# Kernel tuning notes

Hardware: AMD Instinct MI355X
Metric: run time of the kernel (lower is better)

Reference implementation:

```python
import jax, jax.numpy as jnp
import numpy as np

B, N = 32, 320          # n_graphs, max_num_nodes
MAX_DIST = 10
NUM_HEADS = 8
AVG_DEG = 8.0


def setup_inputs() -> dict:
    key = jax.random.key(0)
    k1, k2, k3 = jax.random.split(key, 3)
    # random sparse symmetric adjacency, no self loops
    a = jax.random.uniform(k1, (B, N, N)) < (AVG_DEG / N)
    adj = (a | jnp.swapaxes(a, 1, 2)) & ~jnp.eye(N, dtype=bool)[None]
    num_nodes = jax.random.randint(k2, (B,), N // 2 + 1, N + 1).astype(jnp.int32)
    emb_table = jax.random.normal(k3, (MAX_DIST + 2, NUM_HEADS), dtype=jnp.float32)
    emb_table = emb_table.at[0].set(0.0)  # padding_idx=0 (dist == -1 rows)
    return {"adj": adj, "num_nodes": num_nodes, "emb_table": emb_table}


def _batched_apsp(adj, num_nodes, max_dist):
    """Batched all-pairs shortest path distance via parallel frontier BFS.

    adj: [B,N,N] bool, num_nodes: [B] int. Returns dist [B,N,N] int32 with
    -1 for unreachable/padded pairs; reachable dists > max_dist are set to
    max_dist (equivalent after the clamp in the spatial encoder).
    """
    Bn, Nn, _ = adj.shape
    valid = jnp.arange(Nn)[None, :] < num_nodes[:, None]        # [B,N]
    pair = valid[:, :, None] & valid[:, None, :]                # [B,N,N]
    adj = adj & pair
    eye = jnp.eye(Nn, dtype=bool)[None] & pair
    dist = jnp.where(eye, 0, jnp.where(adj, 1, -1)).astype(jnp.int32)
    reach = adj | eye                                           # within dist<=1
    adj_f = adj.astype(jnp.float32)
    for k in range(2, max_dist + 1):
        new_reach = (jnp.matmul(reach.astype(jnp.float32), adj_f) > 0) | reach
        dist = jnp.where(new_reach & ~reach, k, dist)
        reach = new_reach
    # full reachability via distance doubling (handles dist > max_dist)
    full = reach
    steps = int(np.ceil(np.log2(max(Nn / max(max_dist, 1), 2.0))))
    for _ in range(steps):
        f = full.astype(jnp.float32)
        full = jnp.matmul(f, f) > 0
    full = full & pair
    dist = jnp.where(full & (dist < 0), max_dist, dist)
    return jnp.where(pair, dist, -1)


def reference(adj, num_nodes, emb_table):
    dist = _batched_apsp(adj, num_nodes, MAX_DIST)
    # SpatialEncoder: embedding_table(clamp(dist, -1, max_dist) + 1)
    idx = jnp.clip(dist, -1, MAX_DIST) + 1                      # [B,N,N] in [0, max_dist+1]
    return emb_table[idx]                                       # [B,N,N,num_heads]
```

## Files before the change

kernel.cpp:

```cpp
#include <hip/hip_runtime.h>
#include <stdint.h>

typedef unsigned long long u64;
typedef unsigned int u32;
typedef unsigned char u8;

#define Bn 32
#define Nn 320
#define WPN 5
#define ROWW 6
#define MAXD 10
#define NH 8
#define ADJP_WORDS (Bn * Nn * ROWW)
#define CH 8
#define NCHUNK (Nn / CH)
#define TPB 128
#define ESTR 12
#define IDXSTR 336
#define MASK20 ((1u << 20) - 1u)

template<int CTRL> __device__ __forceinline__ u64 ror_or64(u64 v) {
    u32 lo = (u32)v, hi = (u32)(v >> 32);
    lo |= (u32)__builtin_amdgcn_update_dpp(0, (int)lo, CTRL, 0xF, 0xF, true);
    hi |= (u32)__builtin_amdgcn_update_dpp(0, (int)hi, CTRL, 0xF, 0xF, true);
    return ((u64)hi << 32) | lo;
}
template<int CTRL> __device__ __forceinline__ int ror_add(int v) {
    return v + __builtin_amdgcn_update_dpp(0, v, CTRL, 0xF, 0xF, true);
}
#define ROW_ROR_1 0x121
#define ROW_ROR_2 0x122
#define ROW_ROR_4 0x124
#define ROW_ROR_8 0x128

__device__ __forceinline__ bool detect_byte_mode(const u32* a32) {
    int lane = threadIdx.x & 63;
    u32 or0 = 0, or1 = 0;
    #pragma unroll
    for (int k = 0; k < 16; ++k) {
        u32 v = a32[lane + k * 64];
        or0 |= v & 0x000000FFu;
        or1 |= v & 0x0000FF00u;
    }
    bool a0 = __any(or0 != 0);
    bool a1 = __any(or1 != 0);
    return a0 && a1;
}

__global__ __launch_bounds__(256) void build_adj(
        const u8* __restrict__ a8,
        const int* __restrict__ nn_,
        u64* __restrict__ adjW) {
    bool bytemode = detect_byte_mode((const u32*)a8);
    int t = blockIdx.x * blockDim.x + threadIdx.x;
    if (t >= ADJP_WORDS) return;
    int w = t % ROWW;
    int j = (t / ROWW) % Nn;
    int b = t / (ROWW * Nn);
    int nn = nn_[b];
    u64 bits = 0ull;
    if (w < WPN && j < nn) {
        int jbase = w * 64;
        int lim = nn - jbase; if (lim > 64) lim = 64;
        if (lim > 0) {
            long base = ((long)(b * Nn + j)) * Nn + jbase;
            if (bytemode) {
                const uint4* p = (const uint4*)(a8 + base);
                #pragma unroll
                for (int v = 0; v < 4; ++v) {
                    uint4 x = p[v];
                    u32 n0 = ((x.x & 0x01010101u) * 0x01020408u) >> 24;
                    u32 n1 = ((x.y & 0x01010101u) * 0x01020408u) >> 24;
                    u32 n2 = ((x.z & 0x01010101u) * 0x01020408u) >> 24;
                    u32 n3 = ((x.w & 0x01010101u) * 0x01020408u) >> 24;
                    u64 nib = (u64)((n0 & 0xF) | ((n1 & 0xF) << 4) |
                                    ((n2 & 0xF) << 8) | ((n3 & 0xF) << 12));
                    bits |= nib << (v * 16);
                }
            } else {
                const uint4* p = (const uint4*)(((const u32*)a8) + base);
                #pragma unroll
                for (int v = 0; v < 16; ++v) {
                    uint4 x = p[v];
                    u64 nib = (u64)((x.x != 0u) | ((x.y != 0u) << 1) |
                                    ((x.z != 0u) << 2) | ((x.w != 0u) << 3));
                    bits |= nib << (v * 4);
                }
            }
            if (lim < 64) bits &= (1ull << lim) - 1ull;
        }
    }
    adjW[t] = bits;
}

__global__ __launch_bounds__(TPB) void bfs_write(
        const u64* __restrict__ adjW,
        const int* __restrict__ nn_,
        const float* __restrict__ emb,
        float4* __restrict__ out4) {
    int blk = blockIdx.x;
    int b = blk / NCHUNK, chunk = blk % NCHUNK;
    int t = threadIdx.x;
    int wv = t >> 6;
    int lane = t & 63;
    int s = lane >> 4;
    int k = lane & 15;
    int r = wv * 4 + s;

    __shared__ __align__(16) u64 adj_s[Nn * ROWW];
    __shared__ __align__(16) u8 idx_s[CH][IDXSTR];
    __shared__ float emb_s[(MAXD + 2) * ESTR];

    if (t < 96) emb_s[(t >> 3) * ESTR + (t & 7)] = emb[t];

    {
        const uint4* g4 = (const uint4*)(adjW + (size_t)b * (Nn * ROWW));
        uint4* d4 = (uint4*)adj_s;
        #pragma unroll
        for (int it = 0; it < 8; ++it) {
            int i = it * TPB + t;
            if (i < 960) d4[i] = g4[i];
        }
    }
    #pragma unroll
    for (int it = 0; it < 6; ++it) {
        int i = it * TPB + t;
        if (i < 672) ((u32*)idx_s)[i] = 0;
    }
    int nn = nn_[b];
    __syncthreads();

    u64 valid[WPN];
    #pragma unroll
    for (int w = 0; w < WPN; ++w) {
        int c = nn - w * 64;
        valid[w] = (c >= 64) ? ~0ull : ((c <= 0) ? 0ull : ((1ull << c) - 1ull));
    }
    int sg = chunk * CH + r;
    u64 cur[WPN] = {0,0,0,0,0}, vis[WPN] = {0,0,0,0,0};
    if (sg < nn) {
        cur[sg >> 6] = 1ull << (sg & 63);
        vis[sg >> 6] = cur[sg >> 6];
        if (k == 0) idx_s[r][sg] = 1;
    }

    int base = 20 * k, w0 = base >> 6, sh = base & 63;
    u8* myseg = &idx_s[r][base];

    int level = 1;
    while (level <= Nn) {
        u64 unv[WPN];
        #pragma unroll
        for (int w = 0; w < WPN; ++w) unv[w] = valid[w] & ~vis[w];
        u32 segf, segu;
        {
            u64 f = cur[w0] >> sh, u = unv[w0] >> sh;
            if (sh > 44) { f |= cur[w0 + 1] << (64 - sh); u |= unv[w0 + 1] << (64 - sh); }
            segf = (u32)f & MASK20; segu = (u32)u & MASK20;
        }
        int fc = __popc(segf), uw = __popc(segu);
        fc = ror_add<ROW_ROR_1>(fc); fc = ror_add<ROW_ROR_2>(fc);
        fc = ror_add<ROW_ROR_4>(fc); fc = ror_add<ROW_ROR_8>(fc);
        uw = ror_add<ROW_ROR_1>(uw); uw = ror_add<ROW_ROR_2>(uw);
        uw = ror_add<ROW_ROR_4>(uw); uw = ror_add<ROW_ROR_8>(uw);
        if (!__any(fc != 0)) break;

        u64 nxt[WPN] = {0,0,0,0,0};
        if (fc > 0 && uw > 0) {
            if (fc <= uw) {
                u32 m = segf;
                while (m) {
                    int j0 = base + __builtin_ctz(m); m &= m - 1;
                    int j1 = j0;
                    if (m) { j1 = base + __builtin_ctz(m); m &= m - 1; }
                    const u64* r0 = adj_s + j0 * ROWW;
                    const u64* r1 = adj_s + j1 * ROWW;
                    ulonglong2 a0 = *(const ulonglong2*)r0;
                    ulonglong2 a1 = *(const ulonglong2*)(r0 + 2);
                    u64 a4 = r0[4];
                    ulonglong2 b0 = *(const ulonglong2*)r1;
                    ulonglong2 b1 = *(const ulonglong2*)(r1 + 2);
                    u64 b4 = r1[4];
                    nxt[0] |= a0.x | b0.x; nxt[1] |= a0.y | b0.y;
                    nxt[2] |= a1.x | b1.x; nxt[3] |= a1.y | b1.y;
                    nxt[4] |= a4 | b4;
                }
            } else {
                u32 m = segu;
                while (m) {
                    int p0 = __builtin_ctz(m); m &= m - 1;
                    int p1 = p0; bool h = (m != 0u);
                    if (h) { p1 = __builtin_ctz(m); m &= m - 1; }
                    int j0 = base + p0, j1 = base + p1;
                    const u64* r0 = adj_s + j0 * ROWW;
                    const u64* r1 = adj_s + j1 * ROWW;
                    ulonglong2 a0 = *(const ulonglong2*)r0;
                    ulonglong2 a1 = *(const ulonglong2*)(r0 + 2);
                    u64 a4 = r0[4];
                    ulonglong2 b0 = *(const ulonglong2*)r1;
                    ulonglong2 b1 = *(const ulonglong2*)(r1 + 2);
                    u64 b4 = r1[4];
                    u64 t0 = (a0.x & cur[0]) | (a0.y & cur[1]) | (a1.x & cur[2]) |
                             (a1.y & cur[3]) | (a4 & cur[4]);
                    u64 t1 = (b0.x & cur[0]) | (b0.y & cur[1]) | (b1.x & cur[2]) |
                             (b1.y & cur[3]) | (b4 & cur[4]);
                    if (t0) nxt[j0 >> 6] |= 1ull << (j0 & 63);
                    if (h && t1) nxt[j1 >> 6] |= 1ull << (j1 & 63);
                }
            }
            #pragma unroll
            for (int w = 0; w < WPN; ++w) {
                u64 v = nxt[w];
                v = ror_or64<ROW_ROR_1>(v);
                v = ror_or64<ROW_ROR_2>(v);
                v = ror_or64<ROW_ROR_4>(v);
                v = ror_or64<ROW_ROR_8>(v);
                nxt[w] = v & unv[w];
            }
            u64 any = nxt[0] | nxt[1] | nxt[2] | nxt[3] | nxt[4];
            if (any) {
                u8 val = (u8)((level < MAXD ? level : MAXD) + 1);
                u64 f = nxt[w0] >> sh;
                if (sh > 44) f |= nxt[w0 + 1] << (64 - sh);
                u32 segn = (u32)f & MASK20;
                while (segn) { int p = __builtin_ctz(segn); segn &= segn - 1; myseg[p] = val; }
                #pragma unroll
                for (int w = 0; w < WPN; ++w) vis[w] |= nxt[w];
            }
        }
        #pragma unroll
        for (int w = 0; w < WPN; ++w) cur[w] = nxt[w];
        ++level;
    }

    float4* gout = out4 + (size_t)(b * Nn + chunk * CH) * (Nn * NH / 4);
    #pragma unroll
    for (int r2 = 0; r2 < 4; ++r2) {
        int rr = wv * 4 + r2;
        const u8* irow = idx_s[rr];
        float4* rowout = gout + rr * (Nn * NH / 4);
        #pragma unroll
        for (int i = 0; i < 10; ++i) {
            int f = i * 64 + lane;
            int e = irow[f >> 1];
            const float* ep = emb_s + e * ESTR + ((f & 1) << 2);
            rowout[f] = *(const float4*)ep;
        }
    }
}

extern "C" void kernel_launch(void* const* d_in, const int* in_sizes, int n_in,
                              void* d_out, int out_size, void* d_ws, size_t ws_size,
                              hipStream_t stream) {
    const u8*    adj = (const u8*)d_in[0];
    const int*   nn  = (const int*)d_in[1];
    const float* emb = (const float*)d_in[2];

    u64* adjW = (u64*)d_ws;

    build_adj<<<(ADJP_WORDS + 255) / 256, 256, 0, stream>>>(adj, nn, adjW);
    bfs_write<<<Bn * NCHUNK, TPB, 0, stream>>>(adjW, nn, emb, (float4*)d_out);
}
```

Before: 31.55 us.

## Replace per-source frontier BFS with vertex-parallel multi-source bitmask propagation

The BFS is restructured so that each thread owns one vertex and holds a 20-bit mask recording which of the block's 20 sources have reached it. Each level ORs the masks of the vertex's neighbours, read from a transposed shared adjacency, and a block-wide sync count ends the loop. This replaces the earlier 16-lanes-per-source frontier scheme with push/pull switching and DPP reductions. Blocks grow to 320 threads and the grid shrinks to 16 per graph, so each block does more work and fewer blocks run. The cost is one __syncthreads per level and an irregular neighbour loop per thread.

Result: slower. 34.70 us (+10.0%).

```diff
diff --git a/kernel.cpp b/kernel.cpp
--- a/kernel.cpp
+++ b/kernel.cpp
@@ -8,30 +8,13 @@
 #define Bn 32
 #define Nn 320
 #define WPN 5
-#define ROWW 6
 #define MAXD 10
 #define NH 8
-#define ADJP_WORDS (Bn * Nn * ROWW)
-#define CH 8
-#define NCHUNK (Nn / CH)
-#define TPB 128
+#define CHS 20
+#define NCH (Nn / CHS)
+#define TPB Nn
 #define ESTR 12
-#define IDXSTR 336
-#define MASK20 ((1u << 20) - 1u)
-
-template<int CTRL> __device__ __forceinline__ u64 ror_or64(u64 v) {
-    u32 lo = (u32)v, hi = (u32)(v >> 32);
-    lo |= (u32)__builtin_amdgcn_update_dpp(0, (int)lo, CTRL, 0xF, 0xF, true);
-    hi |= (u32)__builtin_amdgcn_update_dpp(0, (int)hi, CTRL, 0xF, 0xF, true);
-    return ((u64)hi << 32) | lo;
-}
-template<int CTRL> __device__ __forceinline__ int ror_add(int v) {
-    return v + __builtin_amdgcn_update_dpp(0, v, CTRL, 0xF, 0xF, true);
-}
-#define ROW_ROR_1 0x121
-#define ROW_ROR_2 0x122
-#define ROW_ROR_4 0x124
-#define ROW_ROR_8 0x128
+#define ADJ_WORDS (Bn * Nn * WPN)
 
 __device__ __forceinline__ bool detect_byte_mode(const u32* a32) {
     int lane = threadIdx.x & 63;
@@ -53,13 +36,13 @@
         u64* __restrict__ adjW) {
     bool bytemode = detect_byte_mode((const u32*)a8);
     int t = blockIdx.x * blockDim.x + threadIdx.x;
-    if (t >= ADJP_WORDS) return;
-    int w = t % ROWW;
-    int j = (t / ROWW) % Nn;
-    int b = t / (ROWW * Nn);
+    if (t >= ADJ_WORDS) return;
+    int j = t % Nn;
+    int w = (t / Nn) % WPN;
+    int b = t / (Nn * WPN);
     int nn = nn_[b];
     u64 bits = 0ull;
-    if (w < WPN && j < nn) {
+    if (j < nn) {
         int jbase = w * 64;
         int lim = nn - jbase; if (lim > 64) lim = 64;
         if (lim > 0) {
@@ -99,153 +82,83 @@
         const float* __restrict__ emb,
         float4* __restrict__ out4) {
     int blk = blockIdx.x;
-    int b = blk / NCHUNK, chunk = blk % NCHUNK;
+    int b = blk >> 4;
+    int c = blk & 15;
     int t = threadIdx.x;
-    int wv = t >> 6;
-    int lane = t & 63;
-    int s = lane >> 4;
-    int k = lane & 15;
-    int r = wv * 4 + s;
+    int v = t;
 
-    __shared__ __align__(16) u64 adj_s[Nn * ROWW];
-    __shared__ __align__(16) u8 idx_s[CH][IDXSTR];
-    __shared__ float emb_s[(MAXD + 2) * ESTR];
+    __shared__ __align__(16) u64 adj_s[WPN][Nn];
+    __shared__ u32 S[2][Nn];
+    __shared__ u8 idx_s[CHS][Nn];
+    __shared__ __align__(16) float emb_s[(MAXD + 2) * ESTR];
 
-    if (t < 96) emb_s[(t >> 3) * ESTR + (t & 7)] = emb[t];
+    if (t < (MAXD + 2) * NH) emb_s[(t >> 3) * ESTR + (t & 7)] = emb[t];
 
     {
-        const uint4* g4 = (const uint4*)(adjW + (size_t)b * (Nn * ROWW));
+        const uint4* g4 = (const uint4*)(adjW + (size_t)b * (Nn * WPN));
         uint4* d4 = (uint4*)adj_s;
         #pragma unroll
-        for (int it = 0; it < 8; ++it) {
+        for (int it = 0; it < 3; ++it) {
             int i = it * TPB + t;
-            if (i < 960) d4[i] = g4[i];
+            if (i < (Nn * WPN) / 2) d4[i] = g4[i];
         }
     }
     #pragma unroll
-    for (int it = 0; it < 6; ++it) {
-        int i = it * TPB + t;
-        if (i < 672) ((u32*)idx_s)[i] = 0;
-    }
+    for (int it = 0; it < 5; ++it) ((u32*)idx_s)[it * TPB + t] = 0;
+
     int nn = nn_[b];
+    int base = c * CHS;
+
+    u32 init = 0;
+    if (v >= base && v < base + CHS && v < nn) init = 1u << (v - base);
+    S[0][v] = init;
+
+    int vs = nn - base; if (vs > CHS) vs = CHS; if (vs < 0) vs = 0;
+    u32 full = (vs >= CHS) ? ((1u << CHS) - 1u) : ((1u << vs) - 1u);
+
     __syncthreads();
+    if (init) idx_s[v - base][v] = 1;
 
-    u64 valid[WPN];
-    #pragma unroll
-    for (int w = 0; w < WPN; ++w) {
-        int c = nn - w * 64;
-        valid[w] = (c >= 64) ? ~0ull : ((c <= 0) ? 0ull : ((1ull << c) - 1ull));
-    }
-    int sg = chunk * CH + r;
-    u64 cur[WPN] = {0,0,0,0,0}, vis[WPN] = {0,0,0,0,0};
-    if (sg < nn) {
-        cur[sg >> 6] = 1ull << (sg & 63);
-        vis[sg >> 6] = cur[sg >> 6];
-        if (k == 0) idx_s[r][sg] = 1;
+    int p = 0;
+    for (int level = 1; level <= Nn; ++level) {
+        const u32* Sp = S[p];
+        u32 mo = Sp[v];
+        u32 acc = mo;
+        if (mo != full) {
+            #pragma unroll
+            for (int w = 0; w < WPN; ++w) {
+                u64 m = adj_s[w][v];
+                int ubase = w * 64;
+                while (m) {
+                    int u = ubase + (int)__builtin_ctzll(m);
+                    m &= m - 1;
+                    acc |= Sp[u];
+                }
+            }
+        }
+        u32 nw = acc & ~mo;
+        S[p ^ 1][v] = acc;
+        if (nw) {
+            u8 val = (u8)((level < MAXD ? level : MAXD) + 1);
+            u32 m2 = nw;
+            while (m2) {
+                int s2 = (int)__builtin_ctz(m2);
+                m2 &= m2 - 1;
+                idx_s[s2][v] = val;
+            }
+        }
+        if (__syncthreads_count(nw != 0) == 0) break;
+        p ^= 1;
     }
 
-    int base = 20 * k, w0 = base >> 6, sh = base & 63;
-    u8* myseg = &idx_s[r][base];
-
-    int level = 1;
-    while (level <= Nn) {
-        u64 unv[WPN];
-        #pragma unroll
-        for (int w = 0; w < WPN; ++w) unv[w] = valid[w] & ~vis[w];
-        u32 segf, segu;
-        {
-            u64 f = cur[w0] >> sh, u = unv[w0] >> sh;
-            if (sh > 44) { f |= cur[w0 + 1] << (64 - sh); u |= unv[w0 + 1] << (64 - sh); }
-            segf = (u32)f & MASK20; segu = (u32)u & MASK20;
-        }
-        int fc = __popc(segf), uw = __popc(segu);
-        fc = ror_add<ROW_ROR_1>(fc); fc = ror_add<ROW_ROR_2>(fc);
-        fc = ror_add<ROW_ROR_4>(fc); fc = ror_add<ROW_ROR_8>(fc);
-        uw = ror_add<ROW_ROR_1>(uw); uw = ror_add<ROW_ROR_2>(uw);
-        uw = ror_add<ROW_ROR_4>(uw); uw = ror_add<ROW_ROR_8>(uw);
-        if (!__any(fc != 0)) break;
-
-        u64 nxt[WPN] = {0,0,0,0,0};
-        if (fc > 0 && uw > 0) {
-            if (fc <= uw) {
-                u32 m = segf;
-                while (m) {
-                    int j0 = base + __builtin_ctz(m); m &= m - 1;
-                    int j1 = j0;
-                    if (m) { j1 = base + __builtin_ctz(m); m &= m - 1; }
-                    const u64* r0 = adj_s + j0 * ROWW;
-                    const u64* r1 = adj_s + j1 * ROWW;
-                    ulonglong2 a0 = *(const ulonglong2*)r0;
-                    ulonglong2 a1 = *(const ulonglong2*)(r0 + 2);
-                    u64 a4 = r0[4];
-                    ulonglong2 b0 = *(const ulonglong2*)r1;
-                    ulonglong2 b1 = *(const ulonglong2*)(r1 + 2);
-                    u64 b4 = r1[4];
-                    nxt[0] |= a0.x | b0.x; nxt[1] |= a0.y | b0.y;
-                    nxt[2] |= a1.x | b1.x; nxt[3] |= a1.y | b1.y;
-                    nxt[4] |= a4 | b4;
-                }
-            } else {
-                u32 m = segu;
-                while (m) {
-                    int p0 = __builtin_ctz(m); m &= m - 1;
-                    int p1 = p0; bool h = (m != 0u);
-                    if (h) { p1 = __builtin_ctz(m); m &= m - 1; }
-                    int j0 = base + p0, j1 = base + p1;
-                    const u64* r0 = adj_s + j0 * ROWW;
-                    const u64* r1 = adj_s + j1 * ROWW;
-                    ulonglong2 a0 = *(const ulonglong2*)r0;
-                    ulonglong2 a1 = *(const ulonglong2*)(r0 + 2);
-                    u64 a4 = r0[4];
-                    ulonglong2 b0 = *(const ulonglong2*)r1;
-                    ulonglong2 b1 = *(const ulonglong2*)(r1 + 2);
-                    u64 b4 = r1[4];
-                    u64 t0 = (a0.x & cur[0]) | (a0.y & cur[1]) | (a1.x & cur[2]) |
-                             (a1.y & cur[3]) | (a4 & cur[4]);
-                    u64 t1 = (b0.x & cur[0]) | (b0.y & cur[1]) | (b1.x & cur[2]) |
-                             (b1.y & cur[3]) | (b4 & cur[4]);
-                    if (t0) nxt[j0 >> 6] |= 1ull << (j0 & 63);
-                    if (h && t1) nxt[j1 >> 6] |= 1ull << (j1 & 63);
-                }
-            }
-            #pragma unroll
-            for (int w = 0; w < WPN; ++w) {
-                u64 v = nxt[w];
-                v = ror_or64<ROW_ROR_1>(v);
-                v = ror_or64<ROW_ROR_2>(v);
-                v = ror_or64<ROW_ROR_4>(v);
-                v = ror_or64<ROW_ROR_8>(v);
-                nxt[w] = v & unv[w];
-            }
-            u64 any = nxt[0] | nxt[1] | nxt[2] | nxt[3] | nxt[4];
-            if (any) {
-                u8 val = (u8)((level < MAXD ? level : MAXD) + 1);
-                u64 f = nxt[w0] >> sh;
-                if (sh > 44) f |= nxt[w0 + 1] << (64 - sh);
-                u32 segn = (u32)f & MASK20;
-                while (segn) { int p = __builtin_ctz(segn); segn &= segn - 1; myseg[p] = val; }
-                #pragma unroll
-                for (int w = 0; w < WPN; ++w) vis[w] |= nxt[w];
-            }
-        }
-        #pragma unroll
-        for (int w = 0; w < WPN; ++w) cur[w] = nxt[w];
-        ++level;
-    }
-
-    float4* gout = out4 + (size_t)(b * Nn + chunk * CH) * (Nn * NH / 4);
+    float4* gout = out4 + (size_t)(b * Nn + base) * (Nn * NH / 4);
     #pragma unroll
-    for (int r2 = 0; r2 < 4; ++r2) {
-        int rr = wv * 4 + r2;
-        const u8* irow = idx_s[rr];
-        float4* rowout = gout + rr * (Nn * NH / 4);
-        #pragma unroll
-        for (int i = 0; i < 10; ++i) {
-            int f = i * 64 + lane;
-            int e = irow[f >> 1];
-            const float* ep = emb_s + e * ESTR + ((f & 1) << 2);
-            rowout[f] = *(const float4*)ep;
-        }
+    for (int i = 0; i < 40; ++i) {
+        int r = i >> 1;
+        int f = ((i & 1) ? Nn : 0) + t;
+        int e = idx_s[r][f >> 1];
+        const float* ep = emb_s + e * ESTR + ((f & 1) << 2);
+        gout[r * (Nn * NH / 4) + f] = *(const float4*)ep;
     }
 }
 
@@ -258,6 +171,6 @@
 
     u64* adjW = (u64*)d_ws;
 
-    build_adj<<<(ADJP_WORDS + 255) / 256, 256, 0, stream>>>(adj, nn, adjW);
-    bfs_write<<<Bn * NCHUNK, TPB, 0, stream>>>(adjW, nn, emb, (float4*)d_out);
+    build_adj<<<ADJ_WORDS / 256, 256, 0, stream>>>(adj, nn, adjW);
+    bfs_write<<<Bn * NCH, TPB, 0, stream>>>(adjW, nn, emb, (float4*)d_out);
 }
```
